# Kernel optimization log

Hardware: AMD Instinct MI355X
Metric: run time of the kernel (lower is better)

The kernel has to match this reference:

```python
import jax, jax.numpy as jnp
import numpy as np

H = 64  # LSTM hidden size per direction


def _lstm_dir(x, Wih, Whh, b, reverse):
    # x: [B,T,I]; Wih: [4H,I]; Whh: [4H,H]; b: [4H] (b_ih + b_hh combined)
    if reverse:
        x = x[:, ::-1]
    xg = jnp.einsum('bti,gi->btg', x, Wih) + b  # precompute input gates [B,T,4H]
    B = x.shape[0]
    WhhT = Whh.T  # [H,4H]

    def step(carry, xt_g):
        h, c = carry
        g = xt_g + h @ WhhT  # [B,4H]
        i, f, gg, o = jnp.split(g, 4, axis=-1)  # PyTorch gate order i,f,g,o
        c = jax.nn.sigmoid(f) * c + jax.nn.sigmoid(i) * jnp.tanh(gg)
        h = jax.nn.sigmoid(o) * jnp.tanh(c)
        return (h, c), h

    h0 = jnp.zeros((B, H), x.dtype)
    _, hs = jax.lax.scan(step, (h0, h0), jnp.swapaxes(xg, 0, 1))
    hs = jnp.swapaxes(hs, 0, 1)  # [B,T,H]
    if reverse:
        hs = hs[:, ::-1]
    return hs


def _bilstm(x, wih_f, whh_f, b_f, wih_b, whh_b, b_b):
    fwd = _lstm_dir(x, wih_f, whh_f, b_f, False)
    bwd = _lstm_dir(x, wih_b, whh_b, b_b, True)
    return jnp.concatenate([fwd, bwd], axis=-1)  # [B,T,2H]


def setup_inputs() -> dict:
    key = jax.random.key(0)
    ks = jax.random.split(key, 16)
    B, IN = 8192, 20

    def w(k, shape, fan_in):
        return jax.random.normal(k, shape, jnp.float32) * (1.0 / np.sqrt(fan_in))

    inp = {
        'x': jax.random.normal(ks[0], (B, IN), jnp.float32),
        'fc1_w': w(ks[1], (50, IN), IN),
        'fc1_b': jnp.zeros((50,), jnp.float32),
        # rnn1: input_size=1, bidirectional
        'r1_wih_f': w(ks[2], (4 * H, 1), 1),
        'r1_whh_f': w(ks[3], (4 * H, H), H),
        'r1_b_f': jnp.zeros((4 * H,), jnp.float32),
        'r1_wih_b': w(ks[4], (4 * H, 1), 1),
        'r1_whh_b': w(ks[5], (4 * H, H), H),
        'r1_b_b': jnp.zeros((4 * H,), jnp.float32),
        # rnn2: input_size=2H=128, bidirectional
        'r2_wih_f': w(ks[6], (4 * H, 2 * H), 2 * H),
        'r2_whh_f': w(ks[7], (4 * H, H), H),
        'r2_b_f': jnp.zeros((4 * H,), jnp.float32),
        'r2_wih_b': w(ks[8], (4 * H, 2 * H), 2 * H),
        'r2_whh_b': w(ks[9], (4 * H, H), H),
        'r2_b_b': jnp.zeros((4 * H,), jnp.float32),
        'fc2_w': w(ks[10], (1, 2 * H), 2 * H),
        'fc2_b': jnp.zeros((1,), jnp.float32),
    }
    return inp


def reference(x, fc1_w, fc1_b,
              r1_wih_f, r1_whh_f, r1_b_f, r1_wih_b, r1_whh_b, r1_b_b,
              r2_wih_f, r2_whh_f, r2_b_f, r2_wih_b, r2_whh_b, r2_b_b,
              fc2_w, fc2_b):
    h = x @ fc1_w.T + fc1_b            # [B,50]
    h = h[..., None]                   # [B,50,1]
    h = _bilstm(h, r1_wih_f, r1_whh_f, r1_b_f, r1_wih_b, r1_whh_b, r1_b_b)  # [B,50,128]
    h = jnp.repeat(h, 2, axis=1)       # nearest upsample x2 along time -> [B,100,128]
    h = _bilstm(h, r2_wih_f, r2_whh_f, r2_b_f, r2_wih_b, r2_whh_b, r2_b_b)  # [B,100,128]
    out = jnp.tanh(jnp.einsum('btf,of->bto', h, fc2_w) + fc2_b)  # [B,100,1]
    return out
```

## Files before the change

kernel.cpp:

```cpp
#include <hip/hip_runtime.h>
#include <cmath>

#define H1    64
#define T1    50
#define T2    100
#define BATCH 8192
#define NB2   256
#define NTILE 512

typedef __attribute__((ext_vector_type(8))) short s16x8;
typedef __attribute__((ext_vector_type(4))) float f32x4;

#define MFMA16(a,b,c) __builtin_amdgcn_mfma_f32_16x16x32_bf16(a,b,c,0,0,0)

#define S_SIG  (-1.4426950408889634f)
#define S_TANH ( 2.8853900817779268f)

#define OFF_FC1T  ((size_t)0)
#define OFF_XF    ((size_t)1638400)
#define OFF_WA1   ((size_t)(1638400 + 104857600))
#define OFF_WA2HH (OFF_WA1 + 65536)
#define OFF_WA2IH (OFF_WA2HH + 65536)
#define OFF_PART  (OFF_WA2IH + 131072)
#define OFF_BS    (OFF_PART + 6553600)

__device__ __forceinline__ float rcp_(float x) { return __builtin_amdgcn_rcpf(x); }
__device__ __forceinline__ float exp2_(float x) {
#if __has_builtin(__builtin_amdgcn_exp2f)
    return __builtin_amdgcn_exp2f(x);
#else
    return exp2f(x);
#endif
}
__device__ __forceinline__ float sigp_(float e)  { return rcp_(1.f + exp2_(e)); }
__device__ __forceinline__ float tanhp_(float e) { return 1.f - 2.f * rcp_(1.f + exp2_(e)); }
__device__ __forceinline__ float tanhc_(float c) { return tanhp_(S_TANH * c); }
__device__ __forceinline__ float tanh_(float x)  { return tanhc_(x); }

__device__ __forceinline__ unsigned short bf16_rne(float x) {
    unsigned int u = __float_as_uint(x);
    u += 0x7fffu + ((u >> 16) & 1u);
    return (unsigned short)(u >> 16);
}
__device__ __forceinline__ float bf16f(unsigned short h) {
    return __uint_as_float(((unsigned int)h) << 16);
}

__global__ __launch_bounds__(256) void k_pre(
    const float* __restrict__ whh1f, const float* __restrict__ whh1b,
    const float* __restrict__ whh2f, const float* __restrict__ whh2b,
    const float* __restrict__ wih2f, const float* __restrict__ wih2b,
    const float* __restrict__ b2f,   const float* __restrict__ b2b,
    const float* __restrict__ x, const float* __restrict__ fc1w,
    const float* __restrict__ fc1b,
    unsigned short* __restrict__ WA1, unsigned short* __restrict__ WA2HH,
    unsigned short* __restrict__ WA2IH, float* __restrict__ fc1T,
    float* __restrict__ part, float* __restrict__ BS)
{
    __shared__ float wls[1000];
    __shared__ float bls[50];
    int tid = threadIdx.x;
    int blk = blockIdx.x;
    if (blk < 64) {
        int i = blk * 256 + tid;
        if (i < 8192) {
            int a   = i >> 12;
            int r   = i & 4095;
            int dir = r >> 11, rem = r & 2047;
            int mt  = rem >> 7, rem2 = rem & 127;
            int kk  = rem2 >> 6, l = rem2 & 63;
            const float* s_ = a ? (dir ? whh2b : whh2f) : (dir ? whh1b : whh1f);
            unsigned short* d_ = a ? WA2HH : WA1;
            int gate = mt * 16 + (l & 15);
            float sc = ((gate >> 6) == 2) ? S_TANH : S_SIG;
            int k0   = kk * 32 + (l >> 4) * 8;
            const float* p = s_ + gate * 64 + k0;
            unsigned short* q = d_ + (size_t)r * 8;
#pragma unroll
            for (int j = 0; j < 8; ++j) q[j] = bf16_rne(p[j] * sc);
        } else {
            int r   = i - 8192;
            int dir = r >> 12, rem = r & 4095;
            int mt  = rem >> 8, rem2 = rem & 255;
            int kk  = rem2 >> 6, l = rem2 & 63;
            const float* s_ = dir ? wih2b : wih2f;
            int gate = mt * 16 + (l & 15);
            float sc = ((gate >> 6) == 2) ? S_TANH : S_SIG;
            int k0   = kk * 32 + (l >> 4) * 8;
            const float* p = s_ + gate * 128 + k0;
            unsigned short* q = WA2IH + (size_t)r * 8;
#pragma unroll
            for (int j = 0; j < 8; ++j) q[j] = bf16_rne(p[j] * sc);
        }
    } else if (blk < 96) {
        for (int i = tid; i < 1000; i += 256) wls[i] = fc1w[i];
        if (tid < 50) bls[tid] = fc1b[tid];
        __syncthreads();
        int bidx = (blk - 64) * 256 + tid;
        float xv[20];
#pragma unroll
        for (int i = 0; i < 20; ++i) xv[i] = x[bidx * 20 + i];
        for (int t = 0; t < T1; ++t) {
            float s = bls[t];
#pragma unroll
            for (int i = 0; i < 20; ++i) s += xv[i] * wls[t * 20 + i];
            fc1T[t * BATCH + bidx] = s;
        }
    } else if (blk < 352) {
        const int n = 2 * T2 * BATCH;
        for (int i = (blk - 96) * 256 + tid; i < n; i += 256 * 256) part[i] = 0.f;
    } else {
        for (int i = tid; i < 512; i += 256) {
            int d = i >> 8, m = i & 255;
            const float* bb = d ? b2b : b2f;
            float sc = ((m >> 6) == 2) ? S_TANH : S_SIG;
            BS[i] = bb[m] * sc;
        }
    }
}

__global__ __launch_bounds__(512, 4) void k_lstm1(
    const float* __restrict__ wih1f, const float* __restrict__ b1f,
    const float* __restrict__ wih1b, const float* __restrict__ b1b,
    const unsigned short* __restrict__ WA1,
    const float* __restrict__ fc1T,
    unsigned short* __restrict__ XF)
{
    __shared__ float x1s[T1][32];
    __shared__ unsigned short Htf[2][2][2][2][64][8];
    int tid  = threadIdx.x;
    int lane = tid & 63;
    int w    = __builtin_amdgcn_readfirstlane(tid >> 6);
    int wh   = w & 3, wsh = w >> 2;
    int quad = lane >> 4, col = lane & 15;
    int dir  = blockIdx.y, bblk = blockIdx.x;

    for (int i = tid; i < T1 * 32; i += 512) {
        int t = i >> 5, s = i & 31;
        x1s[t][s] = fc1T[t * BATCH + bblk * 32 + s];
    }
    const float* wih = dir ? wih1b : wih1f;
    const float* bia = dir ? b1b : b1f;
    f32x4 wvv[4], bvv[4];
#pragma unroll
    for (int g = 0; g < 4; ++g) {
        float sc = (g == 2) ? S_TANH : S_SIG;
#pragma unroll
        for (int r = 0; r < 4; ++r) {
            int gate = g * 64 + wh * 16 + quad * 4 + r;
            wvv[g][r] = wih[gate] * sc;
            bvv[g][r] = bia[gate] * sc;
        }
    }
    s16x8 whhA[4][2];
#pragma unroll
    for (int g = 0; g < 4; ++g)
#pragma unroll
        for (int kk = 0; kk < 2; ++kk)
            whhA[g][kk] = *(const s16x8*)(WA1 +
                ((size_t)((dir * 16 + (g * 4 + wh)) * 2 + kk) * 64 + lane) * 8);

    float c[4];
#pragma unroll
    for (int r = 0; r < 4; ++r) c[r] = 0.f;

    int lq  = 2 * (wh & 1) + (quad >> 1);
    int lp  = lq * 16 + col;
    int jo  = (quad & 1) * 4;
    int kkw = wh >> 1;
    int kk1 = dir * 2 + (wh >> 1);
    int gtile = bblk * 2 + wsh;
    __syncthreads();
    int buf = 0;
    for (int step = 0; step < T1; ++step) {
        int t = dir ? (T1 - 1 - step) : step;
        float xt = x1s[t][wsh * 16 + col];
        f32x4 acc[4];
#pragma unroll
        for (int g = 0; g < 4; ++g)
#pragma unroll
            for (int r = 0; r < 4; ++r)
                acc[g][r] = bvv[g][r] + wvv[g][r] * xt;
        if (step) {
#pragma unroll
            for (int hf = 0; hf < 2; ++hf) {
                s16x8 hb0 = *(const s16x8*)&Htf[buf][hf][0][wsh][lane][0];
                s16x8 hb1 = *(const s16x8*)&Htf[buf][hf][1][wsh][lane][0];
#pragma unroll
                for (int g = 0; g < 4; ++g) {
                    acc[g] = MFMA16(whhA[g][0], hb0, acc[g]);
                    acc[g] = MFMA16(whhA[g][1], hb1, acc[g]);
                }
            }
        }
        int nbuf = buf ^ 1;
        unsigned short hh[4], hl[4];
#pragma unroll
        for (int r = 0; r < 4; ++r) {
            float cc = sigp_(acc[1][r]) * c[r] + sigp_(acc[0][r]) * tanhp_(acc[2][r]);
            c[r] = cc;
            float h = sigp_(acc[3][r]) * tanhc_(cc);
            hh[r] = bf16_rne(h);
            hl[r] = bf16_rne(h - bf16f(hh[r]));
        }
        uint2 vhi, vlo;
        vhi.x = (unsigned)hh[0] | ((unsigned)hh[1] << 16);
        vhi.y = (unsigned)hh[2] | ((unsigned)hh[3] << 16);
        vlo.x = (unsigned)hl[0] | ((unsigned)hl[1] << 16);
        vlo.y = (unsigned)hl[2] | ((unsigned)hl[3] << 16);
        *(uint2*)&Htf[nbuf][0][kkw][wsh][lp][jo] = vhi;
        *(uint2*)&Htf[nbuf][1][kkw][wsh][lp][jo] = vlo;
        *(uint2*)(XF + ((((size_t)t * 4 + kk1) * NTILE + gtile) * 64 + lp) * 8 + jo) = vhi;
        __syncthreads();
        buf = nbuf;
    }
}

__global__ __launch_bounds__(512, 4) void k_lstm2(
    const float* __restrict__ BS,
    const float* __restrict__ fc2w,
    const unsigned short* __restrict__ WA2HH,
    const unsigned short* __restrict__ WA2IH,
    const unsigned short* __restrict__ XF,
    float* __restrict__ part)
{
    __shared__ unsigned short wAl[16][4][64][8];
    __shared__ unsigned short Htf[2][2][2][2][64][8];
    int tid  = threadIdx.x;
    int lane = tid & 63;
    int w    = __builtin_amdgcn_readfirstlane(tid >> 6);
    int wh   = w & 3, wsh = w >> 2;
    int quad = lane >> 4, col = lane & 15;
    int dir  = blockIdx.y, bblk = blockIdx.x;
    int gtile = bblk * 2 + wsh;

    {
        const uint4* src = (const uint4*)(WA2IH + (size_t)dir * 32768);
        uint4* dst = (uint4*)&wAl[0][0][0][0];
        for (int i = tid; i < 4096; i += 512) dst[i] = src[i];
    }
    float f2v[4];
#pragma unroll
    for (int r = 0; r < 4; ++r)
        f2v[r] = fc2w[dir * 64 + wh * 16 + quad * 4 + r];

    s16x8 whhA[4][2];
#pragma unroll
    for (int g = 0; g < 4; ++g)
#pragma unroll
        for (int kk = 0; kk < 2; ++kk)
            whhA[g][kk] = *(const s16x8*)(WA2HH +
                ((size_t)((dir * 16 + (g * 4 + wh)) * 2 + kk) * 64 + lane) * 8);

    const float4* bsp = (const float4*)(BS + dir * 256 + wh * 16 + quad * 4);

    float c[4];
#pragma unroll
    for (int r = 0; r < 4; ++r) c[r] = 0.f;

    int lq  = 2 * (wh & 1) + (quad >> 1);
    int lp  = lq * 16 + col;
    int jo  = (quad & 1) * 4;
    int kkw = wh >> 1;

    s16x8 xbC[4], xbN[4];
    {
        int tp0 = dir ? (T1 - 1) : 0;
#pragma unroll
        for (int kk = 0; kk < 4; ++kk)
            xbC[kk] = *(const s16x8*)(XF +
                (((size_t)(tp0 * 4 + kk) * NTILE + gtile) * 64 + lane) * 8);
    }
    f32x4 xacc[4];
    __syncthreads();
    int buf = 0;

    for (int step = 0; step < T2; ++step) {
        int t2 = dir ? (T2 - 1 - step) : step;
        if ((step & 1) == 0) {
#pragma unroll
            for (int g = 0; g < 4; ++g) {
                float4 bv4 = bsp[g * 16];
                f32x4 a; a[0] = bv4.x; a[1] = bv4.y; a[2] = bv4.z; a[3] = bv4.w;
#pragma unroll
                for (int kk = 0; kk < 4; ++kk) {
                    s16x8 wa = *(const s16x8*)&wAl[g * 4 + wh][kk][lane][0];
                    a = MFMA16(wa, xbC[kk], a);
                }
                xacc[g] = a;
            }
            int tp  = t2 >> 1;
            int tpn = dir ? (tp > 0 ? tp - 1 : 0) : (tp < T1 - 1 ? tp + 1 : T1 - 1);
#pragma unroll
            for (int kk = 0; kk < 4; ++kk)
                xbN[kk] = *(const s16x8*)(XF +
                    (((size_t)(tpn * 4 + kk) * NTILE + gtile) * 64 + lane) * 8);
        }
        f32x4 acc[4];
        if (step) {
            s16x8 hb00 = *(const s16x8*)&Htf[buf][0][0][wsh][lane][0];
            s16x8 hb01 = *(const s16x8*)&Htf[buf][0][1][wsh][lane][0];
            s16x8 hb10 = *(const s16x8*)&Htf[buf][1][0][wsh][lane][0];
            s16x8 hb11 = *(const s16x8*)&Htf[buf][1][1][wsh][lane][0];
#pragma unroll
            for (int g = 0; g < 4; ++g) {
                f32x4 a = MFMA16(whhA[g][0], hb00, xacc[g]);
                a = MFMA16(whhA[g][1], hb01, a);
                a = MFMA16(whhA[g][0], hb10, a);
                a = MFMA16(whhA[g][1], hb11, a);
                acc[g] = a;
            }
        } else {
#pragma unroll
            for (int g = 0; g < 4; ++g) acc[g] = xacc[g];
        }
        int nbuf = buf ^ 1;
        unsigned int uhi[4];
        unsigned short hl[4];
        float pacc = 0.f;
#pragma unroll
        for (int r = 0; r < 4; ++r) {
            float cc = sigp_(acc[1][r]) * c[r] + sigp_(acc[0][r]) * tanhp_(acc[2][r]);
            c[r] = cc;
            float h = sigp_(acc[3][r]) * tanhc_(cc);
            pacc += f2v[r] * h;
            unsigned int u = __float_as_uint(h);
            uhi[r] = u & 0xFFFF0000u;
            hl[r]  = bf16_rne(h - __uint_as_float(uhi[r]));
        }
        uint2 vhi, vlo;
        vhi.x = (uhi[0] >> 16) | uhi[1];
        vhi.y = (uhi[2] >> 16) | uhi[3];
        vlo.x = (unsigned)hl[0] | ((unsigned)hl[1] << 16);
        vlo.y = (unsigned)hl[2] | ((unsigned)hl[3] << 16);
        *(uint2*)&Htf[nbuf][0][kkw][wsh][lp][jo] = vhi;
        *(uint2*)&Htf[nbuf][1][kkw][wsh][lp][jo] = vlo;
        pacc += __shfl_xor(pacc, 16);
        pacc += __shfl_xor(pacc, 32);
        if (lane < 16)
            atomicAdd(&part[((size_t)(dir * T2 + t2)) * BATCH + bblk * 32 + wsh * 16 + lane], pacc);
        __syncthreads();
        buf = nbuf;
        if (step & 1) {
#pragma unroll
            for (int kk = 0; kk < 4; ++kk) xbC[kk] = xbN[kk];
        }
    }
}

__global__ __launch_bounds__(256) void k_fc2(const float* __restrict__ part,
                                             const float* __restrict__ fc2b,
                                             float* __restrict__ out) {
    int u = blockIdx.x * 256 + threadIdx.x;
    if (u >= BATCH * T2) return;
    int b = u / T2, t = u - b * T2;
    float p = part[(size_t)t * BATCH + b] + part[((size_t)T2 + t) * BATCH + b] + fc2b[0];
    out[u] = tanh_(p);
}

extern "C" void kernel_launch(void* const* d_in, const int* in_sizes, int n_in,
                              void* d_out, int out_size, void* d_ws, size_t ws_size,
                              hipStream_t stream) {
    const float* x      = (const float*)d_in[0];
    const float* fc1w   = (const float*)d_in[1];
    const float* fc1b   = (const float*)d_in[2];
    const float* r1wihf = (const float*)d_in[3];
    const float* r1whhf = (const float*)d_in[4];
    const float* r1bf   = (const float*)d_in[5];
    const float* r1wihb = (const float*)d_in[6];
    const float* r1whhb = (const float*)d_in[7];
    const float* r1bb   = (const float*)d_in[8];
    const float* r2wihf = (const float*)d_in[9];
    const float* r2whhf = (const float*)d_in[10];
    const float* r2bf   = (const float*)d_in[11];
    const float* r2wihb = (const float*)d_in[12];
    const float* r2whhb = (const float*)d_in[13];
    const float* r2bb   = (const float*)d_in[14];
    const float* fc2w   = (const float*)d_in[15];
    const float* fc2b   = (const float*)d_in[16];
    char* ws   = (char*)d_ws;
    float* out = (float*)d_out;

    float*          fc1T  = (float*)(ws + OFF_FC1T);
    unsigned short* XF    = (unsigned short*)(ws + OFF_XF);
    unsigned short* WA1   = (unsigned short*)(ws + OFF_WA1);
    unsigned short* WA2HH = (unsigned short*)(ws + OFF_WA2HH);
    unsigned short* WA2IH = (unsigned short*)(ws + OFF_WA2IH);
    float*          partp = (float*)(ws + OFF_PART);
    float*          BS    = (float*)(ws + OFF_BS);

    k_pre<<<353, 256, 0, stream>>>(r1whhf, r1whhb, r2whhf, r2whhb, r2wihf, r2wihb,
                                   r2bf, r2bb, x, fc1w, fc1b,
                                   WA1, WA2HH, WA2IH, fc1T, partp, BS);
    dim3 g1(NB2, 2);
    k_lstm1<<<g1, 512, 0, stream>>>(r1wihf, r1bf, r1wihb, r1bb, WA1, fc1T, XF);
    k_lstm2<<<g1, 512, 0, stream>>>(BS, fc2w, WA2HH, WA2IH, XF, partp);
    k_fc2<<<(BATCH * T2 + 255) / 256, 256, 0, stream>>>(partp, fc2b, out);
}
```

Baseline: 383.2 us.

## Shrink LSTM1 blocks to one tile and software-pipeline LSTM2 input projection

k_lstm1 now runs 256-thread blocks covering one 16-sample tile, giving twice as many blocks with smaller syncs. Its global XF store moves after the barrier so it can overlap the next step. k_lstm2 computes the input-gate projection for the next input timestep during odd steps, after the recurrent MFMAs, instead of at the start of even steps. This takes that work off the critical path at the cost of extra accumulator registers. The atomicAdd is also moved after the barrier.

```diff
diff --git a/kernel.cpp b/kernel.cpp
--- a/kernel.cpp
+++ b/kernel.cpp
@@ -5,6 +5,7 @@
 #define T1    50
 #define T2    100
 #define BATCH 8192
+#define NB1   512
 #define NB2   256
 #define NTILE 512
 
@@ -119,25 +120,24 @@
     }
 }
 
-__global__ __launch_bounds__(512, 4) void k_lstm1(
+__global__ __launch_bounds__(256, 4) void k_lstm1(
     const float* __restrict__ wih1f, const float* __restrict__ b1f,
     const float* __restrict__ wih1b, const float* __restrict__ b1b,
     const unsigned short* __restrict__ WA1,
     const float* __restrict__ fc1T,
     unsigned short* __restrict__ XF)
 {
-    __shared__ float x1s[T1][32];
-    __shared__ unsigned short Htf[2][2][2][2][64][8];
+    __shared__ float x1s[T1][16];
+    __shared__ unsigned short Htf[2][2][2][64][8];
     int tid  = threadIdx.x;
     int lane = tid & 63;
-    int w    = __builtin_amdgcn_readfirstlane(tid >> 6);
-    int wh   = w & 3, wsh = w >> 2;
+    int wh   = __builtin_amdgcn_readfirstlane(tid >> 6);
     int quad = lane >> 4, col = lane & 15;
     int dir  = blockIdx.y, bblk = blockIdx.x;
 
-    for (int i = tid; i < T1 * 32; i += 512) {
-        int t = i >> 5, s = i & 31;
-        x1s[t][s] = fc1T[t * BATCH + bblk * 32 + s];
+    for (int i = tid; i < T1 * 16; i += 256) {
+        int t = i >> 4, s = i & 15;
+        x1s[t][s] = fc1T[t * BATCH + bblk * 16 + s];
     }
     const float* wih = dir ? wih1b : wih1f;
     const float* bia = dir ? b1b : b1f;
@@ -169,12 +169,12 @@
     int jo  = (quad & 1) * 4;
     int kkw = wh >> 1;
     int kk1 = dir * 2 + (wh >> 1);
-    int gtile = bblk * 2 + wsh;
+    int gtile = bblk;
     __syncthreads();
     int buf = 0;
     for (int step = 0; step < T1; ++step) {
         int t = dir ? (T1 - 1 - step) : step;
-        float xt = x1s[t][wsh * 16 + col];
+        float xt = x1s[t][col];
         f32x4 acc[4];
 #pragma unroll
         for (int g = 0; g < 4; ++g)
@@ -184,8 +184,8 @@
         if (step) {
 #pragma unroll
             for (int hf = 0; hf < 2; ++hf) {
-                s16x8 hb0 = *(const s16x8*)&Htf[buf][hf][0][wsh][lane][0];
-                s16x8 hb1 = *(const s16x8*)&Htf[buf][hf][1][wsh][lane][0];
+                s16x8 hb0 = *(const s16x8*)&Htf[buf][hf][0][lane][0];
+                s16x8 hb1 = *(const s16x8*)&Htf[buf][hf][1][lane][0];
 #pragma unroll
                 for (int g = 0; g < 4; ++g) {
                     acc[g] = MFMA16(whhA[g][0], hb0, acc[g]);
@@ -208,10 +208,10 @@
         vhi.y = (unsigned)hh[2] | ((unsigned)hh[3] << 16);
         vlo.x = (unsigned)hl[0] | ((unsigned)hl[1] << 16);
         vlo.y = (unsigned)hl[2] | ((unsigned)hl[3] << 16);
-        *(uint2*)&Htf[nbuf][0][kkw][wsh][lp][jo] = vhi;
-        *(uint2*)&Htf[nbuf][1][kkw][wsh][lp][jo] = vlo;
+        *(uint2*)&Htf[nbuf][0][kkw][lp][jo] = vhi;
+        *(uint2*)&Htf[nbuf][1][kkw][lp][jo] = vlo;
+        __syncthreads();
         *(uint2*)(XF + ((((size_t)t * 4 + kk1) * NTILE + gtile) * 64 + lp) * 8 + jo) = vhi;
-        __syncthreads();
         buf = nbuf;
     }
 }
@@ -263,39 +263,38 @@
     int jo  = (quad & 1) * 4;
     int kkw = wh >> 1;
 
-    s16x8 xbC[4], xbN[4];
+    s16x8 xbN[4];
     {
         int tp0 = dir ? (T1 - 1) : 0;
 #pragma unroll
         for (int kk = 0; kk < 4; ++kk)
-            xbC[kk] = *(const s16x8*)(XF +
+            xbN[kk] = *(const s16x8*)(XF +
                 (((size_t)(tp0 * 4 + kk) * NTILE + gtile) * 64 + lane) * 8);
     }
-    f32x4 xacc[4];
     __syncthreads();
+    f32x4 xaccC[4], xaccN[4];
+#pragma unroll
+    for (int g = 0; g < 4; ++g) {
+        float4 bv4 = bsp[g * 16];
+        f32x4 a; a[0] = bv4.x; a[1] = bv4.y; a[2] = bv4.z; a[3] = bv4.w;
+#pragma unroll
+        for (int kk = 0; kk < 4; ++kk) {
+            s16x8 wa = *(const s16x8*)&wAl[g * 4 + wh][kk][lane][0];
+            a = MFMA16(wa, xbN[kk], a);
+        }
+        xaccC[g] = a;
+    }
+    {
+        int tp1 = dir ? (T1 - 2) : 1;
+#pragma unroll
+        for (int kk = 0; kk < 4; ++kk)
+            xbN[kk] = *(const s16x8*)(XF +
+                (((size_t)(tp1 * 4 + kk) * NTILE + gtile) * 64 + lane) * 8);
+    }
     int buf = 0;
 
     for (int step = 0; step < T2; ++step) {
         int t2 = dir ? (T2 - 1 - step) : step;
-        if ((step & 1) == 0) {
-#pragma unroll
-            for (int g = 0; g < 4; ++g) {
-                float4 bv4 = bsp[g * 16];
-                f32x4 a; a[0] = bv4.x; a[1] = bv4.y; a[2] = bv4.z; a[3] = bv4.w;
-#pragma unroll
-                for (int kk = 0; kk < 4; ++kk) {
-                    s16x8 wa = *(const s16x8*)&wAl[g * 4 + wh][kk][lane][0];
-                    a = MFMA16(wa, xbC[kk], a);
-                }
-                xacc[g] = a;
-            }
-            int tp  = t2 >> 1;
-            int tpn = dir ? (tp > 0 ? tp - 1 : 0) : (tp < T1 - 1 ? tp + 1 : T1 - 1);
-#pragma unroll
-            for (int kk = 0; kk < 4; ++kk)
-                xbN[kk] = *(const s16x8*)(XF +
-                    (((size_t)(tpn * 4 + kk) * NTILE + gtile) * 64 + lane) * 8);
-        }
         f32x4 acc[4];
         if (step) {
             s16x8 hb00 = *(const s16x8*)&Htf[buf][0][0][wsh][lane][0];
@@ -304,7 +303,7 @@
             s16x8 hb11 = *(const s16x8*)&Htf[buf][1][1][wsh][lane][0];
 #pragma unroll
             for (int g = 0; g < 4; ++g) {
-                f32x4 a = MFMA16(whhA[g][0], hb00, xacc[g]);
+                f32x4 a = MFMA16(whhA[g][0], hb00, xaccC[g]);
                 a = MFMA16(whhA[g][1], hb01, a);
                 a = MFMA16(whhA[g][0], hb10, a);
                 a = MFMA16(whhA[g][1], hb11, a);
@@ -312,7 +311,27 @@
             }
         } else {
 #pragma unroll
-            for (int g = 0; g < 4; ++g) acc[g] = xacc[g];
+            for (int g = 0; g < 4; ++g) acc[g] = xaccC[g];
+        }
+        if ((step & 1) && step < T2 - 1) {
+            int pn = (step >> 1) + 1;
+#pragma unroll
+            for (int g = 0; g < 4; ++g) {
+                float4 bv4 = bsp[g * 16];
+                f32x4 a; a[0] = bv4.x; a[1] = bv4.y; a[2] = bv4.z; a[3] = bv4.w;
+#pragma unroll
+                for (int kk = 0; kk < 4; ++kk) {
+                    s16x8 wa = *(const s16x8*)&wAl[g * 4 + wh][kk][lane][0];
+                    a = MFMA16(wa, xbN[kk], a);
+                }
+                xaccN[g] = a;
+            }
+            int pn2 = (pn + 1 < T1) ? pn + 1 : T1 - 1;
+            int tpn2 = dir ? (T1 - 1 - pn2) : pn2;
+#pragma unroll
+            for (int kk = 0; kk < 4; ++kk)
+                xbN[kk] = *(const s16x8*)(XF +
+                    (((size_t)(tpn2 * 4 + kk) * NTILE + gtile) * 64 + lane) * 8);
         }
         int nbuf = buf ^ 1;
         unsigned int uhi[4];
@@ -337,14 +356,14 @@
         *(uint2*)&Htf[nbuf][1][kkw][wsh][lp][jo] = vlo;
         pacc += __shfl_xor(pacc, 16);
         pacc += __shfl_xor(pacc, 32);
+        __syncthreads();
         if (lane < 16)
             atomicAdd(&part[((size_t)(dir * T2 + t2)) * BATCH + bblk * 32 + wsh * 16 + lane], pacc);
-        __syncthreads();
+        if (step & 1) {
+#pragma unroll
+            for (int g = 0; g < 4; ++g) xaccC[g] = xaccN[g];
+        }
         buf = nbuf;
-        if (step & 1) {
-#pragma unroll
-            for (int kk = 0; kk < 4; ++kk) xbC[kk] = xbN[kk];
-        }
     }
 }
 
@@ -392,8 +411,9 @@
     k_pre<<<353, 256, 0, stream>>>(r1whhf, r1whhb, r2whhf, r2whhb, r2wihf, r2wihb,
                                    r2bf, r2bb, x, fc1w, fc1b,
                                    WA1, WA2HH, WA2IH, fc1T, partp, BS);
-    dim3 g1(NB2, 2);
-    k_lstm1<<<g1, 512, 0, stream>>>(r1wihf, r1bf, r1wihb, r1bb, WA1, fc1T, XF);
-    k_lstm2<<<g1, 512, 0, stream>>>(BS, fc2w, WA2HH, WA2IH, XF, partp);
+    dim3 gl1(NB1, 2);
+    k_lstm1<<<gl1, 256, 0, stream>>>(r1wihf, r1bf, r1wihb, r1bb, WA1, fc1T, XF);
+    dim3 gl2(NB2, 2);
+    k_lstm2<<<gl2, 512, 0, stream>>>(BS, fc2w, WA2HH, WA2IH, XF, partp);
     k_fc2<<<(BATCH * T2 + 255) / 256, 256, 0, stream>>>(partp, fc2b, out);
 }
```

Measured after the change: 414.2 us. 1.08x slower.
